# Kernel optimization log

Hardware: AMD Instinct MI355X
Metric: run time of the kernel (lower is better)

The kernel has to match this reference:

```python
import jax, jax.numpy as jnp
import numpy as np

B, T, D_IN, H, NC = 256, 512, 40, 128, 7


def _lstm_dir(x, W_ih, W_hh, b):
    # x: [B,T,D]; W_ih: [4H,D]; W_hh: [4H,H]; b: [4H] (b_ih+b_hh combined)
    pre = jnp.einsum('btd,gd->btg', x, W_ih) + b  # [B,T,4H]
    h0 = jnp.zeros((x.shape[0], W_hh.shape[1]), x.dtype)
    c0 = jnp.zeros_like(h0)

    def step(carry, p_t):
        h, c = carry
        g = p_t + h @ W_hh.T  # [B,4H]
        i, f, gg, o = jnp.split(g, 4, axis=-1)  # PyTorch gate order: i,f,g,o
        i = jax.nn.sigmoid(i)
        f = jax.nn.sigmoid(f)
        gg = jnp.tanh(gg)
        o = jax.nn.sigmoid(o)
        c = f * c + i * gg
        h = o * jnp.tanh(c)
        return (h, c), h

    _, hs = jax.lax.scan(step, (h0, c0), jnp.swapaxes(pre, 0, 1))  # [T,B,H]
    return jnp.swapaxes(hs, 0, 1)  # [B,T,H]


def _bilstm_layer(x, Wf, Uf, bf, Wr, Ur, br):
    fwd = _lstm_dir(x, Wf, Uf, bf)
    rev = _lstm_dir(x[:, ::-1], Wr, Ur, br)[:, ::-1]
    return jnp.concatenate([fwd, rev], axis=-1)  # [B,T,2H]


def setup_inputs() -> dict:
    key = jax.random.key(0)
    ks = jax.random.split(key, 20)
    s = 1.0 / np.sqrt(H)  # PyTorch LSTM init scale

    def u(k, shape):
        return jax.random.uniform(k, shape, jnp.float32, -s, s)

    inp = {
        'x': jax.random.normal(ks[0], (B, T, D_IN), jnp.float32),
        # layer 0 (input dim 40)
        'W_ih_l0_f': u(ks[1], (4 * H, D_IN)), 'W_hh_l0_f': u(ks[2], (4 * H, H)), 'b_l0_f': u(ks[3], (4 * H,)),
        'W_ih_l0_r': u(ks[4], (4 * H, D_IN)), 'W_hh_l0_r': u(ks[5], (4 * H, H)), 'b_l0_r': u(ks[6], (4 * H,)),
        # layer 1 (input dim 2H)
        'W_ih_l1_f': u(ks[7], (4 * H, 2 * H)), 'W_hh_l1_f': u(ks[8], (4 * H, H)), 'b_l1_f': u(ks[9], (4 * H,)),
        'W_ih_l1_r': u(ks[10], (4 * H, 2 * H)), 'W_hh_l1_r': u(ks[11], (4 * H, H)), 'b_l1_r': u(ks[12], (4 * H,)),
        # classifier head
        'fc_w': u(ks[13], (NC, 2 * H)), 'fc_b': u(ks[14], (NC,)),
    }
    return inp


def reference(x, W_ih_l0_f, W_hh_l0_f, b_l0_f, W_ih_l0_r, W_hh_l0_r, b_l0_r,
              W_ih_l1_f, W_hh_l1_f, b_l1_f, W_ih_l1_r, W_hh_l1_r, b_l1_r,
              fc_w, fc_b):
    h1 = _bilstm_layer(x, W_ih_l0_f, W_hh_l0_f, b_l0_f, W_ih_l0_r, W_hh_l0_r, b_l0_r)
    h2 = _bilstm_layer(h1, W_ih_l1_f, W_hh_l1_f, b_l1_f, W_ih_l1_r, W_hh_l1_r, b_l1_r)
    last = h2[:, -1, :]  # [B,2H]; dropout is identity at eval time
    return last @ fc_w.T + fc_b  # [B,NC]
```

## Files before the change

### kernel.cpp

```cpp
#include <hip/hip_runtime.h>
#include <hip/hip_bf16.h>

typedef short short8 __attribute__((ext_vector_type(8)));
typedef short short4v __attribute__((ext_vector_type(4)));
typedef float f32x4 __attribute__((ext_vector_type(4)));
typedef __bf16 bf16x8 __attribute__((ext_vector_type(8)));

#define DEVI static __device__ __forceinline__

#if __has_builtin(__builtin_amdgcn_exp2f)
#define EXP2(x) __builtin_amdgcn_exp2f(x)
#else
#define EXP2(x) exp2f(x)
#endif
#if __has_builtin(__builtin_amdgcn_rcpf)
#define RCP(x) __builtin_amdgcn_rcpf(x)
#else
#define RCP(x) (1.0f / (x))
#endif

static constexpr int BB = 256, TT = 512, DIN0 = 40, HH = 128, NCLS = 7;
static constexpr int NB = 16;
static constexpr int NTHR = 512;
static constexpr float L2E = 1.44269504088896f;

DEVI short f2b(float x) {
  union { __hip_bfloat16 h; short s; } u;
  u.h = __float2bfloat16(x);
  return u.s;
}

DEVI bf16x8 as_bf(short8 s) { return __builtin_bit_cast(bf16x8, s); }

DEVI void bar_lgkm() {
  asm volatile("s_waitcnt lgkmcnt(0)" ::: "memory");
  __builtin_amdgcn_s_barrier();
  __builtin_amdgcn_sched_barrier(0);
}

template <bool IS_L0>
__global__ __launch_bounds__(NTHR, 2) void lstm2(
    const float* __restrict__ x0, const short* __restrict__ h1_in,
    const float* __restrict__ Wih_f, const float* __restrict__ Whh_f,
    const float* __restrict__ bias_f, const float* __restrict__ Wih_r,
    const float* __restrict__ Whh_r, const float* __restrict__ bias_r,
    short* __restrict__ h1_out, float* __restrict__ h2last) {
  constexpr int K0 = IS_L0 ? 64 : 256;
  constexpr int DI = IS_L0 ? DIN0 : 256;
  constexpr int KFX = K0 / 32;
  constexpr int KFH = HH / 32;
  constexpr int RSH = 136;
  constexpr int XROWB_L0 = 144;
  constexpr int XBUF = IS_L0 ? (16 * XROWB_L0) : 8192;

  __shared__ short Hb[2][NB][RSH];
  __shared__ char Xraw[2 * XBUF];

  const int tid = threadIdx.x;
  const int w = tid >> 6;
  const int lane = tid & 63;
  const int lg = lane >> 4;
  const int bcol = lane & 15;
  const int dir = blockIdx.x & 1;
  const int b0 = (blockIdx.x >> 1) * NB;

  const float* __restrict__ Wih = dir ? Wih_r : Wih_f;
  const float* __restrict__ Whh = dir ? Whh_r : Whh_f;
  const float* __restrict__ bias = dir ? bias_r : bias_f;

  auto tmap = [&](int s) { return dir ? (TT - 1 - s) : s; };

  short8 wx[4][KFX];
  short8 wh[4][KFH];
#pragma unroll
  for (int q = 0; q < 4; ++q) {
    const float scale = (q == 2) ? (2.0f * L2E) : (-L2E);
    const int m = q * HH + w * 16 + bcol;
#pragma unroll
    for (int kk = 0; kk < KFX; ++kk) {
      short8 f;
#pragma unroll
      for (int e = 0; e < 8; ++e) {
        const int k = kk * 32 + lg * 8 + e;
        float v = (k < DI) ? Wih[(size_t)m * DI + k] : 0.0f;
        f[e] = f2b(v * scale);
      }
      wx[q][kk] = f;
    }
#pragma unroll
    for (int kk = 0; kk < KFH; ++kk) {
      short8 f;
#pragma unroll
      for (int e = 0; e < 8; ++e)
        f[e] = f2b(Whh[(size_t)m * HH + kk * 32 + lg * 8 + e] * scale);
      wh[q][kk] = f;
    }
  }

  f32x4 bq[4];
#pragma unroll
  for (int q = 0; q < 4; ++q) {
    const float scale = (q == 2) ? (2.0f * L2E) : (-L2E);
#pragma unroll
    for (int r = 0; r < 4; ++r)
      bq[q][r] = bias[q * HH + w * 16 + lg * 4 + r] * scale;
  }

  for (int i = tid; i < (int)(2 * NB * RSH * 2) / 4; i += NTHR)
    ((int*)&Hb[0][0][0])[i] = 0;
  for (int i = tid; i < (int)(2 * XBUF) / 4; i += NTHR) ((int*)Xraw)[i] = 0;
  __syncthreads();

  auto ldx = [&](int p, int kk) -> short8 {
    if constexpr (IS_L0) {
      return *(const short8*)(Xraw + p * XBUF + bcol * XROWB_L0 + kk * 64 + lg * 16);
    } else {
      int byte = ((bcol << 9) + (kk << 6) + (lg << 4)) ^ ((bcol & 7) << 4);
      return *(const short8*)(Xraw + p * XBUF + byte);
    }
  };

  const int xr0 = tid / 10, c40 = tid % 10;
  const int o_swz = (tid << 4) ^ (((tid >> 5) & 7) << 4);
  const int xr1 = tid >> 5;
  const int xcb = o_swz & 511;
  f32x4 xstage_f = {0.f, 0.f, 0.f, 0.f};
  short8 xstage_h = {0, 0, 0, 0, 0, 0, 0, 0};

  if constexpr (IS_L0) {
    if (tid < 160) {
#pragma unroll
      for (int p = 0; p < 2; ++p) {
        f32x4 v = *(const f32x4*)(x0 + ((size_t)(b0 + xr0) * TT + tmap(p)) * DI + c40 * 4);
        short4v o4;
        o4[0] = f2b(v[0]); o4[1] = f2b(v[1]); o4[2] = f2b(v[2]); o4[3] = f2b(v[3]);
        *(short4v*)(Xraw + p * XBUF + xr0 * XROWB_L0 + c40 * 8) = o4;
      }
      xstage_f = *(const f32x4*)(x0 + ((size_t)(b0 + xr0) * TT + tmap(2)) * DI + c40 * 4);
    }
  } else {
#pragma unroll
    for (int p = 0; p < 2; ++p) {
      short8 v = *(const short8*)((const char*)h1_in +
                  ((((size_t)(b0 + xr1)) * TT + tmap(p)) << 9) + xcb);
      *(short8*)(Xraw + p * XBUF + tid * 16) = v;
    }
    xstage_h = *(const short8*)((const char*)h1_in +
                ((((size_t)(b0 + xr1)) * TT + tmap(2)) << 9) + xcb);
  }
  __syncthreads();

  f32x4 acc[4] = {bq[0], bq[1], bq[2], bq[3]};
#pragma unroll
  for (int kk = 0; kk < KFX; ++kk) {
    const bf16x8 bx = as_bf(ldx(0, kk));
#pragma unroll
    for (int q = 0; q < 4; ++q)
      acc[q] = __builtin_amdgcn_mfma_f32_16x16x32_bf16(as_bf(wx[q][kk]), bx, acc[q], 0, 0, 0);
  }
  __syncthreads();

  f32x4 cst = {0.f, 0.f, 0.f, 0.f};
  const int j0 = w * 16 + lg * 4;

  for (int s = 0; s < TT; ++s) {
    const int cur = s & 1;

    if constexpr (IS_L0) {
      if (tid < 160) {
        if (s + 2 < TT) {
          short4v o4;
          o4[0] = f2b(xstage_f[0]); o4[1] = f2b(xstage_f[1]);
          o4[2] = f2b(xstage_f[2]); o4[3] = f2b(xstage_f[3]);
          *(short4v*)(Xraw + cur * XBUF + xr0 * XROWB_L0 + c40 * 8) = o4;
        }
        if (s + 3 < TT)
          xstage_f = *(const f32x4*)(x0 + ((size_t)(b0 + xr0) * TT + tmap(s + 3)) * DI + c40 * 4);
      }
    } else {
      if (s + 2 < TT) *(short8*)(Xraw + cur * XBUF + tid * 16) = xstage_h;
      if (s + 3 < TT)
        xstage_h = *(const short8*)((const char*)h1_in +
                    ((((size_t)(b0 + xr1)) * TT + tmap(s + 3)) << 9) + xcb);
    }

#pragma unroll
    for (int kk = 0; kk < KFH; ++kk) {
      const bf16x8 bh = as_bf(*(const short8*)&Hb[cur][bcol][kk * 32 + lg * 8]);
#pragma unroll
      for (int q = 0; q < 4; ++q)
        acc[q] = __builtin_amdgcn_mfma_f32_16x16x32_bf16(as_bf(wh[q][kk]), bh, acc[q], 0, 0, 0);
    }

    short4v hp;
    f32x4 hf;
#pragma unroll
    for (int r = 0; r < 4; ++r) {
      const float ig = RCP(1.0f + EXP2(acc[0][r]));
      const float fg = RCP(1.0f + EXP2(acc[1][r]));
      float tg = EXP2(acc[2][r]);
      tg = 1.0f - 2.0f * RCP(tg + 1.0f);
      const float og = RCP(1.0f + EXP2(acc[3][r]));
      const float cn = fg * cst[r] + ig * tg;
      cst[r] = cn;
      float tc = EXP2(cn * (2.0f * L2E));
      tc = 1.0f - 2.0f * RCP(tc + 1.0f);
      const float hv = og * tc;
      hf[r] = hv;
      hp[r] = f2b(hv);
    }
    *(short4v*)&Hb[cur ^ 1][bcol][j0] = hp;

    if constexpr (IS_L0) {
      *(short4v*)(h1_out + (((size_t)(b0 + bcol) * TT + tmap(s)) * 256) + dir * HH + j0) = hp;
    } else {
      if ((dir == 0 && s == TT - 1) || (dir == 1 && s == 0))
        *(f32x4*)(h2last + (size_t)(b0 + bcol) * 256 + dir * HH + j0) = hf;
    }

    if (s + 1 < TT) {
      f32x4 a0 = bq[0], a1 = bq[1], a2 = bq[2], a3 = bq[3];
#pragma unroll
      for (int kk = 0; kk < KFX; ++kk) {
        const bf16x8 bx = as_bf(ldx(cur ^ 1, kk));
        a0 = __builtin_amdgcn_mfma_f32_16x16x32_bf16(as_bf(wx[0][kk]), bx, a0, 0, 0, 0);
        a1 = __builtin_amdgcn_mfma_f32_16x16x32_bf16(as_bf(wx[1][kk]), bx, a1, 0, 0, 0);
        a2 = __builtin_amdgcn_mfma_f32_16x16x32_bf16(as_bf(wx[2][kk]), bx, a2, 0, 0, 0);
        a3 = __builtin_amdgcn_mfma_f32_16x16x32_bf16(as_bf(wx[3][kk]), bx, a3, 0, 0, 0);
      }
      acc[0] = a0; acc[1] = a1; acc[2] = a2; acc[3] = a3;
    }

    bar_lgkm();
  }
}

__global__ void fc_kernel(const float* __restrict__ h2last,
                          const float* __restrict__ fcw,
                          const float* __restrict__ fcb,
                          float* __restrict__ out) {
  const int gid = blockIdx.x * blockDim.x + threadIdx.x;
  if (gid >= BB * NCLS) return;
  const int b = gid / NCLS, n = gid % NCLS;
  const float* hp = h2last + (size_t)b * 256;
  const float* wp = fcw + (size_t)n * 256;
  float s = fcb[n];
#pragma unroll 8
  for (int j = 0; j < 256; ++j) s = fmaf(hp[j], wp[j], s);
  out[gid] = s;
}

extern "C" void kernel_launch(void* const* d_in, const int* in_sizes, int n_in,
                              void* d_out, int out_size, void* d_ws, size_t ws_size,
                              hipStream_t stream) {
  const float* x     = (const float*)d_in[0];
  const float* Wih0f = (const float*)d_in[1];
  const float* Whh0f = (const float*)d_in[2];
  const float* b0f   = (const float*)d_in[3];
  const float* Wih0r = (const float*)d_in[4];
  const float* Whh0r = (const float*)d_in[5];
  const float* b0r   = (const float*)d_in[6];
  const float* Wih1f = (const float*)d_in[7];
  const float* Whh1f = (const float*)d_in[8];
  const float* b1f   = (const float*)d_in[9];
  const float* Wih1r = (const float*)d_in[10];
  const float* Whh1r = (const float*)d_in[11];
  const float* b1r   = (const float*)d_in[12];
  const float* fcw   = (const float*)d_in[13];
  const float* fcb   = (const float*)d_in[14];

  short* h1 = (short*)d_ws;
  float* h2last = (float*)((char*)d_ws + (size_t)BB * TT * 256 * 2);

  lstm2<true><<<dim3(32), dim3(NTHR), 0, stream>>>(
      x, nullptr, Wih0f, Whh0f, b0f, Wih0r, Whh0r, b0r, h1, nullptr);
  lstm2<false><<<dim3(32), dim3(NTHR), 0, stream>>>(
      nullptr, h1, Wih1f, Whh1f, b1f, Wih1r, Whh1r, b1r, nullptr, h2last);
  fc_kernel<<<dim3((BB * NCLS + 255) / 256), dim3(256), 0, stream>>>(
      h2last, fcw, fcb, (float*)d_out);
}
```

Measured before the change: 1.156 ms.

## Restructure LSTM step loop: direct global x loads, batched reciprocals, unrolled steps

In layer 0, x is now loaded from global memory straight into registers in MFMA fragment layout, and the input projection for step s+1 is issued before the recurrent MFMAs of step s. This removes the LDS staging buffer for x. The per-element gate reciprocals are replaced by a batched inverse that needs one RCP per four values, with exp inputs clamped to avoid overflow. The hidden-state LDS buffer is relaid out as [k-chunk][batch][8] so each lane reads its fragment as one vector, and the time loop is unrolled by two with fixed buffer indices. The batched inverse adds multiplies and may cost some precision, and every lane now performs its own global x loads.

```diff
diff --git a/kernel.cpp b/kernel.cpp
--- a/kernel.cpp
+++ b/kernel.cpp
@@ -38,9 +38,24 @@
   __builtin_amdgcn_sched_barrier(0);
 }
 
+DEVI f32x4 inv4(f32x4 d) {
+  float p1 = d[0] * d[1];
+  float p2 = p1 * d[2];
+  float p3 = p2 * d[3];
+  float R = RCP(p3);
+  f32x4 r;
+  r[3] = R * p2;
+  float R2 = R * d[3];
+  r[2] = R2 * p1;
+  float R1 = R2 * d[2];
+  r[1] = R1 * d[0];
+  r[0] = R1 * d[1];
+  return r;
+}
+
 template <bool IS_L0>
-__global__ __launch_bounds__(NTHR, 2) void lstm2(
-    const float* __restrict__ x0, const short* __restrict__ h1_in,
+__global__ __launch_bounds__(NTHR, 2) void lstm3(
+    const float* __restrict__ xg, const short* __restrict__ xb,
     const float* __restrict__ Wih_f, const float* __restrict__ Whh_f,
     const float* __restrict__ bias_f, const float* __restrict__ Wih_r,
     const float* __restrict__ Whh_r, const float* __restrict__ bias_r,
@@ -48,13 +63,10 @@
   constexpr int K0 = IS_L0 ? 64 : 256;
   constexpr int DI = IS_L0 ? DIN0 : 256;
   constexpr int KFX = K0 / 32;
-  constexpr int KFH = HH / 32;
-  constexpr int RSH = 136;
-  constexpr int XROWB_L0 = 144;
-  constexpr int XBUF = IS_L0 ? (16 * XROWB_L0) : 8192;
-
-  __shared__ short Hb[2][NB][RSH];
-  __shared__ char Xraw[2 * XBUF];
+  constexpr int XB = IS_L0 ? 64 : 16384;
+
+  __shared__ short Hb2[2][16][16][8];
+  __shared__ char Xraw[XB];
 
   const int tid = threadIdx.x;
   const int w = tid >> 6;
@@ -63,6 +75,7 @@
   const int bcol = lane & 15;
   const int dir = blockIdx.x & 1;
   const int b0 = (blockIdx.x >> 1) * NB;
+  const int j0 = w * 16 + lg * 4;
 
   const float* __restrict__ Wih = dir ? Wih_r : Wih_f;
   const float* __restrict__ Whh = dir ? Whh_r : Whh_f;
@@ -71,7 +84,7 @@
   auto tmap = [&](int s) { return dir ? (TT - 1 - s) : s; };
 
   short8 wx[4][KFX];
-  short8 wh[4][KFH];
+  short8 wh[4][4];
 #pragma unroll
   for (int q = 0; q < 4; ++q) {
     const float scale = (q == 2) ? (2.0f * L2E) : (-L2E);
@@ -88,7 +101,7 @@
       wx[q][kk] = f;
     }
 #pragma unroll
-    for (int kk = 0; kk < KFH; ++kk) {
+    for (int kk = 0; kk < 4; ++kk) {
       short8 f;
 #pragma unroll
       for (int e = 0; e < 8; ++e)
@@ -106,132 +119,161 @@
       bq[q][r] = bias[q * HH + w * 16 + lg * 4 + r] * scale;
   }
 
-  for (int i = tid; i < (int)(2 * NB * RSH * 2) / 4; i += NTHR)
-    ((int*)&Hb[0][0][0])[i] = 0;
-  for (int i = tid; i < (int)(2 * XBUF) / 4; i += NTHR) ((int*)Xraw)[i] = 0;
+  for (int i = tid; i < (int)sizeof(Hb2) / 4; i += NTHR) ((int*)&Hb2[0][0][0][0])[i] = 0;
   __syncthreads();
 
-  auto ldx = [&](int p, int kk) -> short8 {
-    if constexpr (IS_L0) {
-      return *(const short8*)(Xraw + p * XBUF + bcol * XROWB_L0 + kk * 64 + lg * 16);
-    } else {
-      int byte = ((bcol << 9) + (kk << 6) + (lg << 4)) ^ ((bcol & 7) << 4);
-      return *(const short8*)(Xraw + p * XBUF + byte);
-    }
-  };
-
-  const int xr0 = tid / 10, c40 = tid % 10;
-  const int o_swz = (tid << 4) ^ (((tid >> 5) & 7) << 4);
-  const int xr1 = tid >> 5;
-  const int xcb = o_swz & 511;
-  f32x4 xstage_f = {0.f, 0.f, 0.f, 0.f};
-  short8 xstage_h = {0, 0, 0, 0, 0, 0, 0, 0};
-
-  if constexpr (IS_L0) {
-    if (tid < 160) {
-#pragma unroll
-      for (int p = 0; p < 2; ++p) {
-        f32x4 v = *(const f32x4*)(x0 + ((size_t)(b0 + xr0) * TT + tmap(p)) * DI + c40 * 4);
-        short4v o4;
-        o4[0] = f2b(v[0]); o4[1] = f2b(v[1]); o4[2] = f2b(v[2]); o4[3] = f2b(v[3]);
-        *(short4v*)(Xraw + p * XBUF + xr0 * XROWB_L0 + c40 * 8) = o4;
-      }
-      xstage_f = *(const f32x4*)(x0 + ((size_t)(b0 + xr0) * TT + tmap(2)) * DI + c40 * 4);
-    }
-  } else {
-#pragma unroll
-    for (int p = 0; p < 2; ++p) {
-      short8 v = *(const short8*)((const char*)h1_in +
-                  ((((size_t)(b0 + xr1)) * TT + tmap(p)) << 9) + xcb);
-      *(short8*)(Xraw + p * XBUF + tid * 16) = v;
-    }
-    xstage_h = *(const short8*)((const char*)h1_in +
-                ((((size_t)(b0 + xr1)) * TT + tmap(2)) << 9) + xcb);
-  }
-  __syncthreads();
-
-  f32x4 acc[4] = {bq[0], bq[1], bq[2], bq[3]};
-#pragma unroll
-  for (int kk = 0; kk < KFX; ++kk) {
-    const bf16x8 bx = as_bf(ldx(0, kk));
-#pragma unroll
-    for (int q = 0; q < 4; ++q)
-      acc[q] = __builtin_amdgcn_mfma_f32_16x16x32_bf16(as_bf(wx[q][kk]), bx, acc[q], 0, 0, 0);
-  }
-  __syncthreads();
-
   f32x4 cst = {0.f, 0.f, 0.f, 0.f};
-  const int j0 = w * 16 + lg * 4;
-
-  for (int s = 0; s < TT; ++s) {
-    const int cur = s & 1;
-
-    if constexpr (IS_L0) {
-      if (tid < 160) {
-        if (s + 2 < TT) {
-          short4v o4;
-          o4[0] = f2b(xstage_f[0]); o4[1] = f2b(xstage_f[1]);
-          o4[2] = f2b(xstage_f[2]); o4[3] = f2b(xstage_f[3]);
-          *(short4v*)(Xraw + cur * XBUF + xr0 * XROWB_L0 + c40 * 8) = o4;
-        }
-        if (s + 3 < TT)
-          xstage_f = *(const f32x4*)(x0 + ((size_t)(b0 + xr0) * TT + tmap(s + 3)) * DI + c40 * 4);
-      }
-    } else {
-      if (s + 2 < TT) *(short8*)(Xraw + cur * XBUF + tid * 16) = xstage_h;
-      if (s + 3 < TT)
-        xstage_h = *(const short8*)((const char*)h1_in +
-                    ((((size_t)(b0 + xr1)) * TT + tmap(s + 3)) << 9) + xcb);
-    }
-
-#pragma unroll
-    for (int kk = 0; kk < KFH; ++kk) {
-      const bf16x8 bh = as_bf(*(const short8*)&Hb[cur][bcol][kk * 32 + lg * 8]);
-#pragma unroll
-      for (int q = 0; q < 4; ++q)
-        acc[q] = __builtin_amdgcn_mfma_f32_16x16x32_bf16(as_bf(wh[q][kk]), bh, acc[q], 0, 0, 0);
-    }
-
+
+  auto cell = [&](f32x4& a0, f32x4& a1, f32x4& a2, f32x4& a3, int buf, int s) {
+    f32x4 Ei, Ef, Eg, Eo;
+#pragma unroll
+    for (int r = 0; r < 4; ++r) {
+      Ei[r] = EXP2(fminf(a0[r], 30.f));
+      Ef[r] = EXP2(fminf(a1[r], 30.f));
+      Eg[r] = EXP2(fminf(a2[r], 30.f));
+      Eo[r] = EXP2(fminf(a3[r], 30.f));
+    }
+    const f32x4 one = {1.f, 1.f, 1.f, 1.f};
+    f32x4 si = inv4(one + Ei), sf = inv4(one + Ef);
+    f32x4 gd = inv4(one + Eg), so = inv4(one + Eo);
+    f32x4 Ec;
+#pragma unroll
+    for (int r = 0; r < 4; ++r) {
+      float tg = 1.f - 2.f * gd[r];
+      cst[r] = sf[r] * cst[r] + si[r] * tg;
+      Ec[r] = EXP2(fminf(cst[r] * (2.f * L2E), 30.f));
+    }
+    f32x4 cd = inv4(one + Ec);
     short4v hp;
     f32x4 hf;
 #pragma unroll
     for (int r = 0; r < 4; ++r) {
-      const float ig = RCP(1.0f + EXP2(acc[0][r]));
-      const float fg = RCP(1.0f + EXP2(acc[1][r]));
-      float tg = EXP2(acc[2][r]);
-      tg = 1.0f - 2.0f * RCP(tg + 1.0f);
-      const float og = RCP(1.0f + EXP2(acc[3][r]));
-      const float cn = fg * cst[r] + ig * tg;
-      cst[r] = cn;
-      float tc = EXP2(cn * (2.0f * L2E));
-      tc = 1.0f - 2.0f * RCP(tc + 1.0f);
-      const float hv = og * tc;
+      float hv = so[r] * (1.f - 2.f * cd[r]);
       hf[r] = hv;
       hp[r] = f2b(hv);
     }
-    *(short4v*)&Hb[cur ^ 1][bcol][j0] = hp;
-
+    *(short4v*)&Hb2[buf ^ 1][j0 >> 3][bcol][j0 & 7] = hp;
     if constexpr (IS_L0) {
-      *(short4v*)(h1_out + (((size_t)(b0 + bcol) * TT + tmap(s)) * 256) + dir * HH + j0) = hp;
+      *(short4v*)(h1_out + (((size_t)(b0 + bcol) * TT + tmap(s)) << 8) + dir * HH + j0) = hp;
     } else {
       if ((dir == 0 && s == TT - 1) || (dir == 1 && s == 0))
-        *(f32x4*)(h2last + (size_t)(b0 + bcol) * 256 + dir * HH + j0) = hf;
-    }
-
-    if (s + 1 < TT) {
-      f32x4 a0 = bq[0], a1 = bq[1], a2 = bq[2], a3 = bq[3];
-#pragma unroll
-      for (int kk = 0; kk < KFX; ++kk) {
-        const bf16x8 bx = as_bf(ldx(cur ^ 1, kk));
-        a0 = __builtin_amdgcn_mfma_f32_16x16x32_bf16(as_bf(wx[0][kk]), bx, a0, 0, 0, 0);
-        a1 = __builtin_amdgcn_mfma_f32_16x16x32_bf16(as_bf(wx[1][kk]), bx, a1, 0, 0, 0);
-        a2 = __builtin_amdgcn_mfma_f32_16x16x32_bf16(as_bf(wx[2][kk]), bx, a2, 0, 0, 0);
-        a3 = __builtin_amdgcn_mfma_f32_16x16x32_bf16(as_bf(wx[3][kk]), bx, a3, 0, 0, 0);
-      }
-      acc[0] = a0; acc[1] = a1; acc[2] = a2; acc[3] = a3;
-    }
-
+        *(f32x4*)(h2last + ((size_t)(b0 + bcol) << 8) + dir * HH + j0) = hf;
+    }
+  };
+
+  if constexpr (IS_L0) {
+    const float* xlane = xg + (size_t)(b0 + bcol) * TT * DI + lg * 8;
+    auto ldxg = [&](f32x4* dst, int sidx) {
+      int ss = (sidx < TT) ? sidx : (TT - 1);
+      const float* p = xlane + (size_t)tmap(ss) * DI;
+      dst[0] = *(const f32x4*)(p);
+      dst[1] = *(const f32x4*)(p + 4);
+      if (lg == 0) {
+        dst[2] = *(const f32x4*)(p + 32);
+        dst[3] = *(const f32x4*)(p + 36);
+      }
+    };
+    auto prefill = [&](f32x4* acc, const f32x4* xr) {
+      short8 f0, f1;
+#pragma unroll
+      for (int e = 0; e < 4; ++e) {
+        f0[e] = f2b(xr[0][e]);
+        f0[4 + e] = f2b(xr[1][e]);
+        f1[e] = f2b(xr[2][e]);
+        f1[4 + e] = f2b(xr[3][e]);
+      }
+      bf16x8 bx0 = as_bf(f0), bx1 = as_bf(f1);
+#pragma unroll
+      for (int q = 0; q < 4; ++q) {
+        acc[q] = __builtin_amdgcn_mfma_f32_16x16x32_bf16(as_bf(wx[q][0]), bx0, bq[q], 0, 0, 0);
+        acc[q] = __builtin_amdgcn_mfma_f32_16x16x32_bf16(as_bf(wx[q][1]), bx1, acc[q], 0, 0, 0);
+      }
+    };
+    auto step = [&](int s, int buf, f32x4* acc, f32x4* accN, f32x4* xR) {
+      prefill(accN, xR);
+#pragma unroll
+      for (int kk = 0; kk < 4; ++kk) {
+        bf16x8 bh = as_bf(*(const short8*)&Hb2[buf][kk * 4 + lg][bcol][0]);
+#pragma unroll
+        for (int q = 0; q < 4; ++q)
+          acc[q] = __builtin_amdgcn_mfma_f32_16x16x32_bf16(as_bf(wh[q][kk]), bh, acc[q], 0, 0, 0);
+      }
+      cell(acc[0], acc[1], acc[2], acc[3], buf, s);
+      ldxg(xR, s + 3);
+      bar_lgkm();
+    };
+
+    const f32x4 z = {0.f, 0.f, 0.f, 0.f};
+    f32x4 xP[4] = {z, z, z, z}, xA[4] = {z, z, z, z}, xB[4] = {z, z, z, z};
+    ldxg(xP, 0);
+    ldxg(xA, 1);
+    ldxg(xB, 2);
+    f32x4 accA[4], accB[4];
+    prefill(accA, xP);
+
+    for (int s = 0; s < TT; s += 2) {
+      step(s, 0, accA, accB, xA);
+      step(s + 1, 1, accB, accA, xB);
+    }
+  } else {
+    const int xr1 = tid >> 5;
+    const int xcb = ((tid << 4) ^ (((tid >> 5) & 7) << 4)) & 511;
+    auto ldx = [&](int p, int kk) -> short8 {
+      int byte = ((bcol << 9) + (kk << 6) + (lg << 4)) ^ ((bcol & 7) << 4);
+      return *(const short8*)(Xraw + p * 8192 + byte);
+    };
+    auto ldg = [&](int sidx) -> short8 {
+      int ss = (sidx < TT) ? sidx : (TT - 1);
+      return *(const short8*)((const char*)xb + ((size_t)(b0 + xr1) * TT + tmap(ss)) * 512 + xcb);
+    };
+
+    {
+      short8 v0 = ldg(0), v1 = ldg(1);
+      *(short8*)(Xraw + tid * 16) = v0;
+      *(short8*)(Xraw + 8192 + tid * 16) = v1;
+    }
+    short8 xstage = ldg(2);
+    __syncthreads();
+
+    f32x4 acc[4];
+#pragma unroll
+    for (int q = 0; q < 4; ++q) acc[q] = bq[q];
+#pragma unroll
+    for (int kk = 0; kk < 8; ++kk) {
+      bf16x8 bx = as_bf(ldx(0, kk));
+#pragma unroll
+      for (int q = 0; q < 4; ++q)
+        acc[q] = __builtin_amdgcn_mfma_f32_16x16x32_bf16(as_bf(wx[q][kk]), bx, acc[q], 0, 0, 0);
+    }
     bar_lgkm();
+
+    auto step = [&](int s, int buf) {
+      *(short8*)(Xraw + buf * 8192 + tid * 16) = xstage;
+      xstage = ldg(s + 3);
+#pragma unroll
+      for (int kk = 0; kk < 4; ++kk) {
+        bf16x8 bh = as_bf(*(const short8*)&Hb2[buf][kk * 4 + lg][bcol][0]);
+#pragma unroll
+        for (int q = 0; q < 4; ++q)
+          acc[q] = __builtin_amdgcn_mfma_f32_16x16x32_bf16(as_bf(wh[q][kk]), bh, acc[q], 0, 0, 0);
+      }
+      cell(acc[0], acc[1], acc[2], acc[3], buf, s);
+#pragma unroll
+      for (int q = 0; q < 4; ++q) acc[q] = bq[q];
+#pragma unroll
+      for (int kk = 0; kk < 8; ++kk) {
+        bf16x8 bx = as_bf(ldx(buf ^ 1, kk));
+#pragma unroll
+        for (int q = 0; q < 4; ++q)
+          acc[q] = __builtin_amdgcn_mfma_f32_16x16x32_bf16(as_bf(wx[q][kk]), bx, acc[q], 0, 0, 0);
+      }
+      bar_lgkm();
+    };
+
+    for (int s = 0; s < TT; s += 2) {
+      step(s, 0);
+      step(s + 1, 1);
+    }
   }
 }
 
@@ -272,9 +314,9 @@
   short* h1 = (short*)d_ws;
   float* h2last = (float*)((char*)d_ws + (size_t)BB * TT * 256 * 2);
 
-  lstm2<true><<<dim3(32), dim3(NTHR), 0, stream>>>(
+  lstm3<true><<<dim3(32), dim3(NTHR), 0, stream>>>(
       x, nullptr, Wih0f, Whh0f, b0f, Wih0r, Whh0r, b0r, h1, nullptr);
-  lstm2<false><<<dim3(32), dim3(NTHR), 0, stream>>>(
+  lstm3<false><<<dim3(32), dim3(NTHR), 0, stream>>>(
       nullptr, h1, Wih1f, Whh1f, b1f, Wih1r, Whh1r, b1r, nullptr, h2last);
   fc_kernel<<<dim3((BB * NCLS + 255) / 256), dim3(256), 0, stream>>>(
       h2last, fcw, fcb, (float*)d_out);
```

New measurement: 1.259 ms. 1.09x slower.
